# Optimization experiments

Measured on AMD Instinct MI355X. Metric: run time of the kernel, lower is better.

Reference implementation:

```python
import jax, jax.numpy as jnp
import numpy as np

K_NEIGHBORS = 50
DELTA = 0.001


def setup_inputs() -> dict:
    key = jax.random.key(0)
    k1, k2, k3 = jax.random.split(key, 3)
    A, N, D, B = 8, 50000, 64, 256
    return {
        "query": jax.random.normal(k1, (B, D), dtype=jnp.float32),
        "mem_keys": jax.random.normal(k2, (A, N, D), dtype=jnp.float32),
        "mem_values": jax.random.normal(k3, (A, N), dtype=jnp.float32),
    }


def reference(query, mem_keys, mem_values):
    # query: [B, D]; mem_keys: [A, N, D]; mem_values: [A, N]
    q_sq = jnp.sum(query ** 2, axis=-1, keepdims=True)  # [B, 1]

    def per_action(keys, values):
        # keys: [N, D], values: [N]
        # brute-force squared-L2 distances (replaces Annoy ANN search)
        d2 = q_sq + jnp.sum(keys ** 2, axis=-1)[None, :] - 2.0 * query @ keys.T  # [B, N]
        _, idx = jax.lax.top_k(-d2, K_NEIGHBORS)  # [B, K] nearest indices
        gk = keys[idx]        # [B, K, D] gathered keys
        gv = values[idx]      # [B, K]    gathered values
        # inverse-distance kernel, exact recompute as in torch forward
        dist = jnp.sum((query[:, None, :] - gk) ** 2, axis=-1)  # [B, K]
        w = 1.0 / (dist + DELTA)
        out = jnp.sum(w * gv, axis=-1) / jnp.sum(w, axis=-1)  # [B]
        return out, idx, dist

    vals, idxs, scores = jax.vmap(per_action)(mem_keys, mem_values)  # [A,B], [A,B,K], [A,B,K]
    values_all = vals.T  # [B, A]
    max_values = jnp.max(values_all, axis=-1, keepdims=True)   # [B, 1]
    actions = jnp.argmax(values_all, axis=-1, keepdims=True)   # [B, 1]
    return (max_values, actions, values_all,
            jnp.transpose(idxs, (1, 0, 2)), jnp.transpose(scores, (1, 0, 2)))
```

## Files before the change

kernel.cpp:

```cpp
#include <hip/hip_runtime.h>
#include <cstdint>


#define A_N 8
#define N_N 50000
#define D_N 64
#define B_N 256
#define K_N 50

constexpr int   QT  = 64;
constexpr int   NBT = 128;
constexpr int   NT  = (N_N + NBT - 1) / NBT;
constexpr int   SL  = 40;
constexpr int   SLF = 64;
constexpr int   SLOTS = 24;
constexpr int   CAPMAX = 4096;
constexpr float TMARG = 25.0f;
constexpr int   NPAD = NT * NBT;

constexpr int OFF_MAX = 0;
constexpr int OFF_ACT = 256;
constexpr int OFF_VAL = 512;
constexpr int OFF_IDX = 2560;
constexpr int OFF_SC  = 104960;

constexpr size_t WSF_CNT  = 0;
constexpr size_t WSF_THR  = 8192;
constexpr size_t WSF_KBF  = 1609728;
constexpr size_t WSF_CAND = 52858880;

constexpr size_t WS_CNT  = 0;
constexpr size_t WS_QSQ  = 16384;
constexpr size_t WS_KSQ  = 17408;
constexpr size_t WS_CAND = 1617920;

typedef __attribute__((ext_vector_type(8))) short bf16x8;
typedef __attribute__((ext_vector_type(4))) float f32x4;

__device__ __forceinline__ unsigned bfr(float f)
{
    unsigned u = __float_as_uint(f);
    return (u + 0x7FFFu + ((u >> 16) & 1u)) >> 16;
}
__device__ __forceinline__ uint4 packbf8(const float* f)
{
    uint4 w;
    w.x = bfr(f[0]) | (bfr(f[1]) << 16);
    w.y = bfr(f[2]) | (bfr(f[3]) << 16);
    w.z = bfr(f[4]) | (bfr(f[5]) << 16);
    w.w = bfr(f[6]) | (bfr(f[7]) << 16);
    return w;
}

__device__ __forceinline__ void async16(void* lds, const void* g)
{
    __builtin_amdgcn_global_load_lds(
        (const __attribute__((address_space(1))) void*)g,
        (__attribute__((address_space(3))) void*)lds, 16, 0, 0);
}

__device__ __forceinline__ float np_tree8(const float r[8])
{
    return __fadd_rn(__fadd_rn(__fadd_rn(r[0], r[1]), __fadd_rn(r[2], r[3])),
                     __fadd_rn(__fadd_rn(r[4], r[5]), __fadd_rn(r[6], r[7])));
}

__device__ __forceinline__ float np_sumsq64(const float* __restrict__ a)
{
    float r[8];
#pragma unroll
    for (int j = 0; j < 8; ++j) r[j] = __fmul_rn(a[j], a[j]);
    for (int i = 8; i < 64; i += 8)
#pragma unroll
        for (int j = 0; j < 8; ++j)
            r[j] = __fadd_rn(r[j], __fmul_rn(a[i + j], a[i + j]));
    return np_tree8(r);
}

__device__ __forceinline__ float np_sum50(const float* __restrict__ a)
{
    float r[8];
#pragma unroll
    for (int j = 0; j < 8; ++j) r[j] = a[j];
    for (int i = 8; i < 48; i += 8)
#pragma unroll
        for (int j = 0; j < 8; ++j) r[j] = __fadd_rn(r[j], a[i + j]);
    float res = np_tree8(r);
    res = __fadd_rn(res, a[48]);
    res = __fadd_rn(res, a[49]);
    return res;
}


__global__ __launch_bounds__(256)
void dnd_k0b(const float* __restrict__ keys, float* __restrict__ thrn,
             uint4* __restrict__ kbf, int* __restrict__ cnt)
{
    __shared__ float khalf[NBT][2];
    const int t   = blockIdx.x;
    const int a   = blockIdx.y;
    const int tid = threadIdx.x;
    const int r   = tid >> 1, h = tid & 1;

    int n = t * NBT + r; if (n > N_N - 1) n = N_N - 1;
    const float4* s4 = (const float4*)(keys + ((size_t)a * N_N + n) * D_N + h * 32);
    float4 fv[8];
#pragma unroll
    for (int i = 0; i < 8; ++i) fv[i] = s4[i];
    float ps = 0.f;
#pragma unroll
    for (int i = 0; i < 8; ++i)
        ps += fv[i].x * fv[i].x + fv[i].y * fv[i].y + fv[i].z * fv[i].z + fv[i].w * fv[i].w;
    khalf[r][h] = ps;

    const float* f = (const float*)fv;
    const int s = r >> 4, m = r & 15;
    uint4* dst = kbf + ((size_t)(a * NT + t) * 16 + (s * 2 + h)) * 64;
#pragma unroll
    for (int g = 0; g < 4; ++g) dst[g * 16 + m] = packbf8(f + g * 8);

    __syncthreads();
    if (tid < NBT) {
        const int nn = t * NBT + tid;
        float thr = __builtin_huge_valf();
        if (nn < N_N) {
            const float ks = khalf[tid][0] + khalf[tid][1];
            thr = 0.5f * (ks - TMARG);
        }
        thrn[(size_t)a * NPAD + t * NBT + tid] = thr;
    }
    if (t == 0) cnt[a * B_N + tid] = 0;
}

__global__ __launch_bounds__(256, 5)
void dnd_k1(const float* __restrict__ query, const uint4* __restrict__ kbf,
            const float* __restrict__ thrn,
            int* __restrict__ cnt, unsigned* __restrict__ cand, int cap)
{
    __shared__ __align__(16) uint4 afrag[4][2][64];
    __shared__ __align__(16) uint4 bfrag[16][64];
    __shared__ float    thrs[NBT];
    __shared__ int      lcnt[QT];
    __shared__ unsigned lbuf[QT][SLOTS];

    const int a    = blockIdx.z;
    const int q0   = blockIdx.y * QT;
    const int sl   = blockIdx.x;
    const int tid  = threadIdx.x;
    const int lane = tid & 63;
    const int wave = tid >> 6;
    const int quad = lane >> 4;
    const int nl   = lane & 15;

    {
        const int r = tid & 63, seg = tid >> 6;
        const float4* s4 = (const float4*)(query + (size_t)(q0 + r) * D_N + seg * 16);
        float4 fv[4];
#pragma unroll
        for (int i = 0; i < 4; ++i) fv[i] = s4[i];
        const float* f = (const float*)fv;
        const int qtile = r >> 4, m = r & 15, kh = seg >> 1;
        const int quadA = (seg & 1) * 2;
        afrag[qtile][kh][quadA * 16 + m]       = packbf8(f);
        afrag[qtile][kh][(quadA + 1) * 16 + m] = packbf8(f + 8);
    }
    if (tid < QT) lcnt[tid] = 0;
    __syncthreads();
    const bf16x8 aA = ((const bf16x8*)afrag)[(wave * 2 + 0) * 64 + lane];
    const bf16x8 aB = ((const bf16x8*)afrag)[(wave * 2 + 1) * 64 + lane];

    int it = 0;
    for (int t = sl; t < NT; t += SL, ++it) {
        const int n0 = t * NBT;
        __syncthreads();
        {
            const char* src = (const char*)(kbf + (size_t)(a * NT + t) * 1024);
#pragma unroll
            for (int i = 0; i < 4; ++i) {
                const int off = i * 4096 + tid * 16;
                async16((char*)bfrag + off, src + off);
            }
        }
        if (tid < NBT) thrs[tid] = thrn[(size_t)a * NPAD + n0 + tid];
        __syncthreads();

#pragma unroll
        for (int s = 0; s < 8; ++s) {
            const bf16x8 b0 = ((const bf16x8*)bfrag)[(s * 2 + 0) * 64 + lane];
            const bf16x8 b1 = ((const bf16x8*)bfrag)[(s * 2 + 1) * 64 + lane];
            f32x4 c = {0.f, 0.f, 0.f, 0.f};
            c = __builtin_amdgcn_mfma_f32_16x16x32_bf16(aA, b0, c, 0, 0, 0);
            c = __builtin_amdgcn_mfma_f32_16x16x32_bf16(aB, b1, c, 0, 0, 0);

            const int   nn  = n0 + s * 16 + nl;
            const float thr = thrs[s * 16 + nl];
#pragma unroll
            for (int r = 0; r < 4; ++r) {
                if (c[r] >= thr) {
                    const int bl = wave * 16 + quad * 4 + r;
                    const float d2rel = fmaf(-2.f, c[r], fmaf(2.f, thr, TMARG));
                    int qv = (int)fmaf(d2rel, 1000.f, 40000.f);
                    qv = qv < 0 ? 0 : (qv > 65535 ? 65535 : qv);
                    const unsigned entry = ((unsigned)qv << 16) | (unsigned)nn;
                    const int p = atomicAdd(&lcnt[bl], 1);
                    if (p < SLOTS) lbuf[bl][p] = entry;
                    else {
                        const int gb = a * B_N + q0 + bl;
                        const int gp = atomicAdd(&cnt[gb], 1);
                        if (gp < cap) cand[(size_t)gb * cap + gp] = entry;
                    }
                }
            }
        }

        const bool last = (t + SL >= NT);
        if ((it & 1) || last) {
            __syncthreads();
            if (tid < QT) {
                int m = lcnt[tid]; lcnt[tid] = 0;
                if (m > SLOTS) m = SLOTS;
                if (m > 0) {
                    const int gb = a * B_N + q0 + tid;
                    const int base = atomicAdd(&cnt[gb], m);
                    unsigned* dst = cand + (size_t)gb * cap;
                    for (int i = 0; i < m; ++i) {
                        const int p = base + i;
                        if (p < cap) dst[p] = lbuf[tid][i];
                    }
                }
            }
        }
    }
}

__global__ __launch_bounds__(256)
void dnd_k2(const float* __restrict__ query, const float* __restrict__ keys,
            const float* __restrict__ values,
            const int* __restrict__ cnt, const unsigned* __restrict__ cand, int cap,
            float* __restrict__ dout)
{
    __shared__ __align__(16) float qrow[D_N];
    __shared__ int   hist[256];
    __shared__ float sdf[512];
    __shared__ int   sn[512];
    __shared__ int   wn[K_N];
    __shared__ float wsc[K_N];
    __shared__ float wgv[K_N];
    __shared__ int   nsurv;
    __shared__ int   bstar;
    __shared__ float qsq_np;

    const int b   = blockIdx.x;
    const int a   = blockIdx.y;
    const int ab  = a * B_N + b;
    const int tid = threadIdx.x;

    if (tid < D_N) qrow[tid] = query[(size_t)b * D_N + tid];
    hist[tid & 255] = 0;
    if (tid == 0) nsurv = 0;
    if (tid < K_N) wn[tid] = 0;
    __syncthreads();
    if (tid == 0) qsq_np = np_sumsq64(qrow);
    __syncthreads();

    int c = cnt[ab]; if (c > cap) c = cap;
    const unsigned* base = cand + (size_t)ab * cap;

    for (int i = tid; i < c; i += 256) {
        int bin = (int)(base[i] >> 16) / 250;
        bin = bin > 255 ? 255 : bin;
        atomicAdd(&hist[bin], 1);
    }
    __syncthreads();
    if (tid == 0) {
        const int need = c < K_N ? c : K_N;
        int cum = 0, bs = 255;
        for (int i = 0; i < 256; ++i) { cum += hist[i]; if (cum >= need) { bs = i; break; } }
        bstar = bs;
    }
    __syncthreads();
    const int bs = bstar + 4;

    for (int i = tid; i < c; i += 256) {
        const unsigned e = base[i];
        int bin = (int)(e >> 16) / 250;
        bin = bin > 255 ? 255 : bin;
        if (bin <= bs) {
            int p = atomicAdd(&nsurv, 1);
            if (p < 512) sn[p] = (int)(e & 0xFFFFu);
        }
    }
    __syncthreads();
    int c2 = nsurv; if (c2 > 512) c2 = 512;

    const float qn = qsq_np;
    for (int i = tid; i < c2; i += 256) {
        const int n = sn[i];
        const float4* kr = (const float4*)(keys + ((size_t)a * N_N + n) * D_N);
        const float4* qr = (const float4*)qrow;
        float r[8];
#pragma unroll
        for (int j = 0; j < 8; ++j) r[j] = 0.f;
        float dot = 0.f;
#pragma unroll
        for (int cch = 0; cch < 16; ++cch) {
            float4 kk = kr[cch]; float4 qv = qr[cch];
            const int j0 = (cch & 1) * 4;
            if (cch < 2) {
                r[j0 + 0] = __fmul_rn(kk.x, kk.x);
                r[j0 + 1] = __fmul_rn(kk.y, kk.y);
                r[j0 + 2] = __fmul_rn(kk.z, kk.z);
                r[j0 + 3] = __fmul_rn(kk.w, kk.w);
            } else {
                r[j0 + 0] = __fadd_rn(r[j0 + 0], __fmul_rn(kk.x, kk.x));
                r[j0 + 1] = __fadd_rn(r[j0 + 1], __fmul_rn(kk.y, kk.y));
                r[j0 + 2] = __fadd_rn(r[j0 + 2], __fmul_rn(kk.z, kk.z));
                r[j0 + 3] = __fadd_rn(r[j0 + 3], __fmul_rn(kk.w, kk.w));
            }
            dot = __fmaf_rn(qv.x, kk.x, dot);
            dot = __fmaf_rn(qv.y, kk.y, dot);
            dot = __fmaf_rn(qv.z, kk.z, dot);
            dot = __fmaf_rn(qv.w, kk.w, dot);
        }
        const float ksq = np_tree8(r);
        sdf[i] = __fsub_rn(__fadd_rn(qn, ksq), __fmul_rn(2.0f, dot));
    }
    __syncthreads();

    for (int i = tid; i < c2; i += 256) {
        const float di = sdf[i]; const int ni = sn[i];
        int rank = 0;
        for (int j = 0; j < c2; ++j) {
            const float dj = sdf[j]; const int nj = sn[j];
            rank += (dj < di || (dj == di && nj < ni)) ? 1 : 0;
        }
        if (rank < K_N) wn[rank] = ni;
    }
    __syncthreads();

    if (tid < K_N) {
        const int n = wn[tid];
        const float* kr = keys + ((size_t)a * N_N + n) * D_N;
        float r[8];
#pragma unroll
        for (int j = 0; j < 8; ++j) {
            float d = __fsub_rn(qrow[j], kr[j]);
            r[j] = __fmul_rn(d, d);
        }
        for (int i = 8; i < 64; i += 8)
#pragma unroll
            for (int j = 0; j < 8; ++j) {
                float d = __fsub_rn(qrow[i + j], kr[i + j]);
                r[j] = __fadd_rn(r[j], __fmul_rn(d, d));
            }
        const float dist = np_tree8(r);
        wsc[tid] = dist;
        wgv[tid] = values[(size_t)a * N_N + n];
        dout[OFF_IDX + (size_t)(b * A_N + a) * K_N + tid] = (float)n;
        dout[OFF_SC  + (size_t)(b * A_N + a) * K_N + tid] = dist;
    }
    __syncthreads();

    if (tid == 0) {
        float w[K_N], wv[K_N];
#pragma unroll
        for (int k = 0; k < K_N; ++k) {
            w[k]  = __fdiv_rn(1.0f, __fadd_rn(wsc[k], 0.001f));
            wv[k] = __fmul_rn(w[k], wgv[k]);
        }
        dout[OFF_VAL + b * A_N + a] = __fdiv_rn(np_sum50(wv), np_sum50(w));
    }
}

__global__ void dnd_k3(float* __restrict__ dout)
{
    const int b = threadIdx.x;
    float best = -__builtin_huge_valf(); int bi = 0;
#pragma unroll
    for (int a = 0; a < A_N; ++a) {
        const float v = dout[OFF_VAL + b * A_N + a];
        if (v > best) { best = v; bi = a; }
    }
    dout[OFF_MAX + b] = best;
    dout[OFF_ACT + b] = (float)bi;
}


__global__ __launch_bounds__(256)
void dnd_k0f(const float* __restrict__ query, const float* __restrict__ keys,
             float* __restrict__ qsq_g, float* __restrict__ ksq_g)
{
    const int r = blockIdx.x * 256 + threadIdx.x;
    if (r >= A_N * N_N + B_N) return;
    const bool isk = r < A_N * N_N;
    const float4* s4 = (const float4*)(isk ? (keys + (size_t)r * D_N)
                                           : (query + (size_t)(r - A_N * N_N) * D_N));
    float s = 0.f;
#pragma unroll
    for (int i = 0; i < 16; ++i) {
        float4 v = s4[i];
        s += v.x * v.x + v.y * v.y + v.z * v.z + v.w * v.w;
    }
    if (isk) ksq_g[r] = s; else qsq_g[r - A_N * N_N] = s;
}

__global__ __launch_bounds__(256, 4)
void dnd_k1f(const float* __restrict__ query, const float* __restrict__ keys,
             const float* __restrict__ qsq_g, const float* __restrict__ ksq_g,
             int* __restrict__ cnt, uint2* __restrict__ cand, int cap)
{
    __shared__ __align__(16) uint4 afrag[4][2][64];
    __shared__ __align__(16) uint4 bfrag[8][2][64];
    __shared__ float qsqs[QT];
    __shared__ float ksqs[NBT];

    const int a    = blockIdx.z;
    const int q0   = blockIdx.y * QT;
    const int sl   = blockIdx.x;
    const int tid  = threadIdx.x;
    const int lane = tid & 63;
    const int wave = tid >> 6;
    const int quad = lane >> 4;
    const int nl   = lane & 15;

    {
        const int r = tid & 63, seg = tid >> 6;
        const float4* s4 = (const float4*)(query + (size_t)(q0 + r) * D_N + seg * 16);
        float4 fv[4];
#pragma unroll
        for (int i = 0; i < 4; ++i) fv[i] = s4[i];
        const float* f = (const float*)fv;
        const int qtile = r >> 4, m = r & 15, kh = seg >> 1;
        const int quadA = (seg & 1) * 2;
        afrag[qtile][kh][quadA * 16 + m]       = packbf8(f);
        afrag[qtile][kh][(quadA + 1) * 16 + m] = packbf8(f + 8);
    }
    if (tid < QT) qsqs[tid] = qsq_g[q0 + tid];

    for (int t = sl; t < NT; t += SLF) {
        const int n0 = t * NBT;
        __syncthreads();
        {
            const int r = tid >> 1, h = tid & 1;
            int n = n0 + r; if (n > N_N - 1) n = N_N - 1;
            const float4* s4 = (const float4*)(keys + ((size_t)a * N_N + n) * D_N + h * 32);
            float4 fv[8];
#pragma unroll
            for (int i = 0; i < 8; ++i) fv[i] = s4[i];
            const float* f = (const float*)fv;
            const int s = r >> 4, m = r & 15;
#pragma unroll
            for (int g = 0; g < 4; ++g)
                bfrag[s][h][g * 16 + m] = packbf8(f + g * 8);
        }
        if (tid < NBT)
            ksqs[tid] = (n0 + tid < N_N) ? ksq_g[(size_t)a * N_N + n0 + tid]
                                         : __builtin_huge_valf();
        __syncthreads();

        const bf16x8 aA = ((const bf16x8*)afrag)[(wave * 2 + 0) * 64 + lane];
        const bf16x8 aB = ((const bf16x8*)afrag)[(wave * 2 + 1) * 64 + lane];

#pragma unroll
        for (int s = 0; s < 8; ++s) {
            const bf16x8 b0 = ((const bf16x8*)bfrag)[(s * 2 + 0) * 64 + lane];
            const bf16x8 b1 = ((const bf16x8*)bfrag)[(s * 2 + 1) * 64 + lane];
            f32x4 c = {0.f, 0.f, 0.f, 0.f};
            c = __builtin_amdgcn_mfma_f32_16x16x32_bf16(aA, b0, c, 0, 0, 0);
            c = __builtin_amdgcn_mfma_f32_16x16x32_bf16(aB, b1, c, 0, 0, 0);

            const int   nn  = n0 + s * 16 + nl;
            const float ksq = ksqs[s * 16 + nl];
#pragma unroll
            for (int r = 0; r < 4; ++r) {
                const int   qr = wave * 16 + quad * 4 + r;
                const float qq = qsqs[qr];
                const float d2 = qq + ksq - 2.0f * c[r];
                if (d2 <= qq + TMARG) {
                    const int b = q0 + qr;
                    const int p = atomicAdd(&cnt[a * B_N + b], 1);
                    if (p < cap) {
                        uint2 e; e.x = __float_as_uint(d2); e.y = (unsigned)nn;
                        cand[(size_t)(a * B_N + b) * cap + p] = e;
                    }
                }
            }
        }
    }
}

__global__ __launch_bounds__(256, 2)
void dnd_k2f(const float* __restrict__ query, const float* __restrict__ keys,
             const float* __restrict__ values,
             const int* __restrict__ cnt, const uint2* __restrict__ cand, int cap,
             float* __restrict__ dout)
{
    __shared__ __align__(16) float qrow[D_N];
    __shared__ float cd[CAPMAX];
    __shared__ int   cn[CAPMAX];
    __shared__ int   hist[256];
    __shared__ float sdf[512];
    __shared__ int   sn[512];
    __shared__ int   wn[K_N];
    __shared__ float wsc[K_N];
    __shared__ float wgv[K_N];
    __shared__ int   nsurv;
    __shared__ int   bstar;
    __shared__ float sqsq;
    __shared__ float qsq_np;

    const int b   = blockIdx.x;
    const int a   = blockIdx.y;
    const int ab  = a * B_N + b;
    const int tid = threadIdx.x;

    if (tid < D_N) qrow[tid] = query[(size_t)b * D_N + tid];
    hist[tid & 255] = 0;
    if (tid == 0) nsurv = 0;
    if (tid < K_N) wn[tid] = 0;
    __syncthreads();
    if (tid < 64) {
        float v = qrow[tid];
        float s = v * v;
#pragma unroll
        for (int m = 1; m < 64; m <<= 1) s += __shfl_xor(s, m, 64);
        if (tid == 0) sqsq = s;
    }
    if (tid == 0) qsq_np = np_sumsq64(qrow);
    __syncthreads();

    int c = cnt[ab]; if (c > cap) c = cap; if (c > CAPMAX) c = CAPMAX;
    const float qq = sqsq;

    for (int i = tid; i < c; i += 256) {
        uint2 e = cand[(size_t)ab * cap + i];
        float d = __uint_as_float(e.x);
        cd[i] = d; cn[i] = (int)e.y;
        int bin = (int)((d - qq + 40.f) * 4.f);
        bin = bin < 0 ? 0 : (bin > 255 ? 255 : bin);
        atomicAdd(&hist[bin], 1);
    }
    __syncthreads();
    if (tid == 0) {
        const int need = c < K_N ? c : K_N;
        int cum = 0, bs = 255;
        for (int i = 0; i < 256; ++i) { cum += hist[i]; if (cum >= need) { bs = i; break; } }
        bstar = bs;
    }
    __syncthreads();
    const int bs = bstar + 4;

    for (int i = tid; i < c; i += 256) {
        float d = cd[i];
        int bin = (int)((d - qq + 40.f) * 4.f);
        bin = bin < 0 ? 0 : (bin > 255 ? 255 : bin);
        if (bin <= bs) {
            int p = atomicAdd(&nsurv, 1);
            if (p < 512) sn[p] = cn[i];
        }
    }
    __syncthreads();
    int c2 = nsurv; if (c2 > 512) c2 = 512;

    const float qn = qsq_np;
    for (int i = tid; i < c2; i += 256) {
        const int n = sn[i];
        const float4* kr = (const float4*)(keys + ((size_t)a * N_N + n) * D_N);
        const float4* qr = (const float4*)qrow;
        float r[8];
#pragma unroll
        for (int j = 0; j < 8; ++j) r[j] = 0.f;
        float dot = 0.f;
#pragma unroll
        for (int cch = 0; cch < 16; ++cch) {
            float4 kk = kr[cch]; float4 qv = qr[cch];
            const int j0 = (cch & 1) * 4;
            if (cch < 2) {
                r[j0 + 0] = __fmul_rn(kk.x, kk.x);
                r[j0 + 1] = __fmul_rn(kk.y, kk.y);
                r[j0 + 2] = __fmul_rn(kk.z, kk.z);
                r[j0 + 3] = __fmul_rn(kk.w, kk.w);
            } else {
                r[j0 + 0] = __fadd_rn(r[j0 + 0], __fmul_rn(kk.x, kk.x));
                r[j0 + 1] = __fadd_rn(r[j0 + 1], __fmul_rn(kk.y, kk.y));
                r[j0 + 2] = __fadd_rn(r[j0 + 2], __fmul_rn(kk.z, kk.z));
                r[j0 + 3] = __fadd_rn(r[j0 + 3], __fmul_rn(kk.w, kk.w));
            }
            dot = __fmaf_rn(qv.x, kk.x, dot);
            dot = __fmaf_rn(qv.y, kk.y, dot);
            dot = __fmaf_rn(qv.z, kk.z, dot);
            dot = __fmaf_rn(qv.w, kk.w, dot);
        }
        const float ksq = np_tree8(r);
        sdf[i] = __fsub_rn(__fadd_rn(qn, ksq), __fmul_rn(2.0f, dot));
    }
    __syncthreads();

    for (int i = tid; i < c2; i += 256) {
        const float di = sdf[i]; const int ni = sn[i];
        int rank = 0;
        for (int j = 0; j < c2; ++j) {
            const float dj = sdf[j]; const int nj = sn[j];
            rank += (dj < di || (dj == di && nj < ni)) ? 1 : 0;
        }
        if (rank < K_N) wn[rank] = ni;
    }
    __syncthreads();

    if (tid < K_N) {
        const int n = wn[tid];
        const float* kr = keys + ((size_t)a * N_N + n) * D_N;
        float r[8];
#pragma unroll
        for (int j = 0; j < 8; ++j) {
            float d = __fsub_rn(qrow[j], kr[j]);
            r[j] = __fmul_rn(d, d);
        }
        for (int i = 8; i < 64; i += 8)
#pragma unroll
            for (int j = 0; j < 8; ++j) {
                float d = __fsub_rn(qrow[i + j], kr[i + j]);
                r[j] = __fadd_rn(r[j], __fmul_rn(d, d));
            }
        const float dist = np_tree8(r);
        wsc[tid] = dist;
        wgv[tid] = values[(size_t)a * N_N + n];
        dout[OFF_IDX + (size_t)(b * A_N + a) * K_N + tid] = (float)n;
        dout[OFF_SC  + (size_t)(b * A_N + a) * K_N + tid] = dist;
    }
    __syncthreads();

    if (tid == 0) {
        float w[K_N], wv[K_N];
#pragma unroll
        for (int k = 0; k < K_N; ++k) {
            w[k]  = __fdiv_rn(1.0f, __fadd_rn(wsc[k], 0.001f));
            wv[k] = __fmul_rn(w[k], wgv[k]);
        }
        dout[OFF_VAL + b * A_N + a] = __fdiv_rn(np_sum50(wv), np_sum50(w));
    }
}

extern "C" void kernel_launch(void* const* d_in, const int* in_sizes, int n_in,
                              void* d_out, int out_size, void* d_ws, size_t ws_size,
                              hipStream_t stream)
{
    (void)in_sizes; (void)n_in; (void)out_size;
    const float* query  = (const float*)d_in[0];
    const float* keys   = (const float*)d_in[1];
    const float* values = (const float*)d_in[2];
    float* dout = (float*)d_out;
    char*  ws   = (char*)d_ws;

    long long capf = 0;
    if (ws_size > WSF_CAND)
        capf = (long long)((ws_size - WSF_CAND) / ((size_t)A_N * B_N * 4));
    const bool full = capf >= 3072;

    if (full) {
        int cap = capf > CAPMAX ? CAPMAX : (int)capf;
        int*      cnt  = (int*)(ws + WSF_CNT);
        float*    thrn = (float*)(ws + WSF_THR);
        uint4*    kbf  = (uint4*)(ws + WSF_KBF);
        unsigned* cand = (unsigned*)(ws + WSF_CAND);

        dim3 g0(NT, A_N);
        dnd_k0b<<<g0, 256, 0, stream>>>(keys, thrn, kbf, cnt);
        dim3 g1(SL, 4, A_N);
        dnd_k1<<<g1, 256, 0, stream>>>(query, kbf, thrn, cnt, cand, cap);
        dim3 g2(B_N, A_N);
        dnd_k2<<<g2, 256, 0, stream>>>(query, keys, values, cnt, cand, cap, dout);
        dnd_k3<<<1, 256, 0, stream>>>(dout);
    } else {
        int*   cnt   = (int*)(ws + WS_CNT);
        float* qsq_g = (float*)(ws + WS_QSQ);
        float* ksq_g = (float*)(ws + WS_KSQ);
        uint2* cand  = (uint2*)(ws + WS_CAND);
        int cap = CAPMAX;
        if (ws_size > WS_CAND) {
            size_t avail = (ws_size - WS_CAND) / ((size_t)A_N * B_N * 8);
            if ((size_t)cap > avail) cap = (int)avail;
        }
        if (cap < 1) cap = 1;

        hipMemsetAsync(cnt, 0, A_N * B_N * sizeof(int), stream);
        dnd_k0f<<<(A_N * N_N + B_N + 255) / 256, 256, 0, stream>>>(query, keys, qsq_g, ksq_g);
        dim3 g1(SLF, 4, A_N);
        dnd_k1f<<<g1, 256, 0, stream>>>(query, keys, qsq_g, ksq_g, cnt, cand, cap);
        dim3 g2(B_N, A_N);
        dnd_k2f<<<g2, 256, 0, stream>>>(query, keys, values, cnt, cand, cap, dout);
        dnd_k3<<<1, 256, 0, stream>>>(dout);
    }
}
```

Before: 270.9 us.

## Process all 256 queries per block in k1 to reuse key tiles

Each k1 block now holds all 256 queries as bf16 MFMA fragments in registers, instead of 64 queries per block across 4 y-blocks. Every key tile loaded from global memory and LDS therefore feeds 4x more MFMAs, and the grid shrinks to 96 slices by 8 actions. The shared arena is reused: the query fragments occupy it first and the per-query candidate buffers later, with fewer slots per query. In exchange, register pressure rises (launch bounds drop to 3 waves), there are fewer blocks, and more candidates may overflow to global atomics.

After: 284.8 us. 5.1% more time.

```diff
diff --git a/kernel.cpp b/kernel.cpp
--- a/kernel.cpp
+++ b/kernel.cpp
@@ -11,9 +11,9 @@
 constexpr int   QT  = 64;
 constexpr int   NBT = 128;
 constexpr int   NT  = (N_N + NBT - 1) / NBT;
-constexpr int   SL  = 40;
+constexpr int   SLQ = 96;
 constexpr int   SLF = 64;
-constexpr int   SLOTS = 24;
+constexpr int   SLOTSQ = 16;
 constexpr int   CAPMAX = 4096;
 constexpr float TMARG = 25.0f;
 constexpr int   NPAD = NT * NBT;
@@ -132,19 +132,20 @@
     if (t == 0) cnt[a * B_N + tid] = 0;
 }
 
-__global__ __launch_bounds__(256, 5)
+__global__ __launch_bounds__(256, 3)
 void dnd_k1(const float* __restrict__ query, const uint4* __restrict__ kbf,
             const float* __restrict__ thrn,
             int* __restrict__ cnt, unsigned* __restrict__ cand, int cap)
 {
-    __shared__ __align__(16) uint4 afrag[4][2][64];
+    __shared__ __align__(16) char arena[16 * 2 * 64 * 16];
     __shared__ __align__(16) uint4 bfrag[16][64];
-    __shared__ float    thrs[NBT];
-    __shared__ int      lcnt[QT];
-    __shared__ unsigned lbuf[QT][SLOTS];
-
-    const int a    = blockIdx.z;
-    const int q0   = blockIdx.y * QT;
+    __shared__ float thrs[NBT];
+    __shared__ int   lcnt[B_N];
+
+    uint4    (*afrag)[2][64]   = (uint4 (*)[2][64])arena;
+    unsigned (*lbuf)[SLOTSQ]   = (unsigned (*)[SLOTSQ])arena;
+
+    const int a    = blockIdx.y;
     const int sl   = blockIdx.x;
     const int tid  = threadIdx.x;
     const int lane = tid & 63;
@@ -154,23 +155,34 @@
 
     {
         const int r = tid & 63, seg = tid >> 6;
-        const float4* s4 = (const float4*)(query + (size_t)(q0 + r) * D_N + seg * 16);
-        float4 fv[4];
-#pragma unroll
-        for (int i = 0; i < 4; ++i) fv[i] = s4[i];
-        const float* f = (const float*)fv;
-        const int qtile = r >> 4, m = r & 15, kh = seg >> 1;
+        const int m = r & 15, kh = seg >> 1;
         const int quadA = (seg & 1) * 2;
-        afrag[qtile][kh][quadA * 16 + m]       = packbf8(f);
-        afrag[qtile][kh][(quadA + 1) * 16 + m] = packbf8(f + 8);
-    }
-    if (tid < QT) lcnt[tid] = 0;
-    __syncthreads();
-    const bf16x8 aA = ((const bf16x8*)afrag)[(wave * 2 + 0) * 64 + lane];
-    const bf16x8 aB = ((const bf16x8*)afrag)[(wave * 2 + 1) * 64 + lane];
+#pragma unroll
+        for (int rep = 0; rep < 4; ++rep) {
+            const int row = rep * 64 + r;
+            const float4* s4 = (const float4*)(query + (size_t)row * D_N + seg * 16);
+            float4 fv[4];
+#pragma unroll
+            for (int i = 0; i < 4; ++i) fv[i] = s4[i];
+            const float* f = (const float*)fv;
+            const int qt16 = rep * 4 + (r >> 4);
+            afrag[qt16][kh][quadA * 16 + m]       = packbf8(f);
+            afrag[qt16][kh][(quadA + 1) * 16 + m] = packbf8(f + 8);
+        }
+    }
+    lcnt[tid] = 0;
+    __syncthreads();
+
+    bf16x8 aF[4][2];
+#pragma unroll
+    for (int sub = 0; sub < 4; ++sub)
+#pragma unroll
+        for (int kh = 0; kh < 2; ++kh)
+            aF[sub][kh] =
+                ((const bf16x8*)afrag)[((wave * 4 + sub) * 2 + kh) * 64 + lane];
 
     int it = 0;
-    for (int t = sl; t < NT; t += SL, ++it) {
+    for (int t = sl; t < NT; t += SLQ, ++it) {
         const int n0 = t * NBT;
         __syncthreads();
         {
@@ -188,39 +200,41 @@
         for (int s = 0; s < 8; ++s) {
             const bf16x8 b0 = ((const bf16x8*)bfrag)[(s * 2 + 0) * 64 + lane];
             const bf16x8 b1 = ((const bf16x8*)bfrag)[(s * 2 + 1) * 64 + lane];
-            f32x4 c = {0.f, 0.f, 0.f, 0.f};
-            c = __builtin_amdgcn_mfma_f32_16x16x32_bf16(aA, b0, c, 0, 0, 0);
-            c = __builtin_amdgcn_mfma_f32_16x16x32_bf16(aB, b1, c, 0, 0, 0);
-
             const int   nn  = n0 + s * 16 + nl;
             const float thr = thrs[s * 16 + nl];
 #pragma unroll
-            for (int r = 0; r < 4; ++r) {
-                if (c[r] >= thr) {
-                    const int bl = wave * 16 + quad * 4 + r;
-                    const float d2rel = fmaf(-2.f, c[r], fmaf(2.f, thr, TMARG));
-                    int qv = (int)fmaf(d2rel, 1000.f, 40000.f);
-                    qv = qv < 0 ? 0 : (qv > 65535 ? 65535 : qv);
-                    const unsigned entry = ((unsigned)qv << 16) | (unsigned)nn;
-                    const int p = atomicAdd(&lcnt[bl], 1);
-                    if (p < SLOTS) lbuf[bl][p] = entry;
-                    else {
-                        const int gb = a * B_N + q0 + bl;
-                        const int gp = atomicAdd(&cnt[gb], 1);
-                        if (gp < cap) cand[(size_t)gb * cap + gp] = entry;
+            for (int sub = 0; sub < 4; ++sub) {
+                f32x4 c = {0.f, 0.f, 0.f, 0.f};
+                c = __builtin_amdgcn_mfma_f32_16x16x32_bf16(aF[sub][0], b0, c, 0, 0, 0);
+                c = __builtin_amdgcn_mfma_f32_16x16x32_bf16(aF[sub][1], b1, c, 0, 0, 0);
+#pragma unroll
+                for (int r = 0; r < 4; ++r) {
+                    if (c[r] >= thr) {
+                        const int bl = (wave * 4 + sub) * 16 + quad * 4 + r;
+                        const float d2rel = fmaf(-2.f, c[r], fmaf(2.f, thr, TMARG));
+                        int qv = (int)fmaf(d2rel, 1000.f, 40000.f);
+                        qv = qv < 0 ? 0 : (qv > 65535 ? 65535 : qv);
+                        const unsigned entry = ((unsigned)qv << 16) | (unsigned)nn;
+                        const int p = atomicAdd(&lcnt[bl], 1);
+                        if (p < SLOTSQ) lbuf[bl][p] = entry;
+                        else {
+                            const int gb = a * B_N + bl;
+                            const int gp = atomicAdd(&cnt[gb], 1);
+                            if (gp < cap) cand[(size_t)gb * cap + gp] = entry;
+                        }
                     }
                 }
             }
         }
 
-        const bool last = (t + SL >= NT);
+        const bool last = (t + SLQ >= NT);
         if ((it & 1) || last) {
             __syncthreads();
-            if (tid < QT) {
+            {
                 int m = lcnt[tid]; lcnt[tid] = 0;
-                if (m > SLOTS) m = SLOTS;
+                if (m > SLOTSQ) m = SLOTSQ;
                 if (m > 0) {
-                    const int gb = a * B_N + q0 + tid;
+                    const int gb = a * B_N + tid;
                     const int base = atomicAdd(&cnt[gb], m);
                     unsigned* dst = cand + (size_t)gb * cap;
                     for (int i = 0; i < m; ++i) {
@@ -666,7 +680,7 @@
 
         dim3 g0(NT, A_N);
         dnd_k0b<<<g0, 256, 0, stream>>>(keys, thrn, kbf, cnt);
-        dim3 g1(SL, 4, A_N);
+        dim3 g1(SLQ, A_N);
         dnd_k1<<<g1, 256, 0, stream>>>(query, kbf, thrn, cnt, cand, cap);
         dim3 g2(B_N, A_N);
         dnd_k2<<<g2, 256, 0, stream>>>(query, keys, values, cnt, cand, cap, dout);
```

## Double-buffer key tiles in candidate kernel and load query fragments into registers

Applied to the files above, without the earlier changes.

The candidate-filter kernel now uses two LDS buffers for key tiles and thresholds. While the current tile is being processed with MFMA, the next tile is prefetched asynchronously into the other buffer, which removes the second barrier per iteration. Query A-fragments are loaded and packed straight into registers instead of going through LDS. Slice count per (action, query-tile) drops from 40 to 32 and occupancy is lowered to 4 blocks per CU, which gives more tiles per block in exchange for the larger LDS footprint and fewer concurrent blocks.

Result: slower. 279.5 us (+3.2%).

```diff
diff --git a/kernel.cpp b/kernel.cpp
--- a/kernel.cpp
+++ b/kernel.cpp
@@ -11,7 +11,7 @@
 constexpr int   QT  = 64;
 constexpr int   NBT = 128;
 constexpr int   NT  = (N_N + NBT - 1) / NBT;
-constexpr int   SL  = 40;
+constexpr int   SL  = 32;
 constexpr int   SLF = 64;
 constexpr int   SLOTS = 24;
 constexpr int   CAPMAX = 4096;
@@ -132,14 +132,13 @@
     if (t == 0) cnt[a * B_N + tid] = 0;
 }
 
-__global__ __launch_bounds__(256, 5)
+__global__ __launch_bounds__(256, 4)
 void dnd_k1(const float* __restrict__ query, const uint4* __restrict__ kbf,
             const float* __restrict__ thrn,
             int* __restrict__ cnt, unsigned* __restrict__ cand, int cap)
 {
-    __shared__ __align__(16) uint4 afrag[4][2][64];
-    __shared__ __align__(16) uint4 bfrag[16][64];
-    __shared__ float    thrs[NBT];
+    __shared__ __align__(16) uint4 bfrag[2][16][64];
+    __shared__ __align__(16) float thrs[2][NBT];
     __shared__ int      lcnt[QT];
     __shared__ unsigned lbuf[QT][SLOTS];
 
@@ -152,48 +151,62 @@
     const int quad = lane >> 4;
     const int nl   = lane & 15;
 
+    bf16x8 aA, aB;
     {
-        const int r = tid & 63, seg = tid >> 6;
-        const float4* s4 = (const float4*)(query + (size_t)(q0 + r) * D_N + seg * 16);
-        float4 fv[4];
-#pragma unroll
-        for (int i = 0; i < 4; ++i) fv[i] = s4[i];
-        const float* f = (const float*)fv;
-        const int qtile = r >> 4, m = r & 15, kh = seg >> 1;
-        const int quadA = (seg & 1) * 2;
-        afrag[qtile][kh][quadA * 16 + m]       = packbf8(f);
-        afrag[qtile][kh][(quadA + 1) * 16 + m] = packbf8(f + 8);
+        const float* qb = query + (size_t)(q0 + wave * 16 + nl) * D_N + quad * 8;
+        float f0[8], f1[8];
+        *(float4*)(f0)     = *(const float4*)(qb);
+        *(float4*)(f0 + 4) = *(const float4*)(qb + 4);
+        *(float4*)(f1)     = *(const float4*)(qb + 32);
+        *(float4*)(f1 + 4) = *(const float4*)(qb + 36);
+        uint4 pa = packbf8(f0), pb = packbf8(f1);
+        aA = *(bf16x8*)&pa;
+        aB = *(bf16x8*)&pb;
     }
     if (tid < QT) lcnt[tid] = 0;
-    __syncthreads();
-    const bf16x8 aA = ((const bf16x8*)afrag)[(wave * 2 + 0) * 64 + lane];
-    const bf16x8 aB = ((const bf16x8*)afrag)[(wave * 2 + 1) * 64 + lane];
-
-    int it = 0;
+
+    {
+        const char* src = (const char*)(kbf + (size_t)(a * NT + sl) * 1024);
+        char* dst = (char*)&bfrag[0][0][0];
+#pragma unroll
+        for (int i = 0; i < 4; ++i) {
+            const int off = i * 4096 + tid * 16;
+            async16(dst + off, src + off);
+        }
+        if (tid < 32)
+            async16((char*)&thrs[0][0] + tid * 16,
+                    (const char*)(thrn + (size_t)a * NPAD + sl * NBT) + tid * 16);
+    }
+
+    int cur = 0, it = 0;
     for (int t = sl; t < NT; t += SL, ++it) {
-        const int n0 = t * NBT;
         __syncthreads();
-        {
-            const char* src = (const char*)(kbf + (size_t)(a * NT + t) * 1024);
+
+        const int tn = t + SL;
+        if (tn < NT) {
+            const char* src = (const char*)(kbf + (size_t)(a * NT + tn) * 1024);
+            char* dst = (char*)&bfrag[cur ^ 1][0][0];
 #pragma unroll
             for (int i = 0; i < 4; ++i) {
                 const int off = i * 4096 + tid * 16;
-                async16((char*)bfrag + off, src + off);
+                async16(dst + off, src + off);
             }
-        }
-        if (tid < NBT) thrs[tid] = thrn[(size_t)a * NPAD + n0 + tid];
-        __syncthreads();
-
+            if (tid < 32)
+                async16((char*)&thrs[cur ^ 1][0] + tid * 16,
+                        (const char*)(thrn + (size_t)a * NPAD + tn * NBT) + tid * 16);
+        }
+
+        const int n0 = t * NBT;
 #pragma unroll
         for (int s = 0; s < 8; ++s) {
-            const bf16x8 b0 = ((const bf16x8*)bfrag)[(s * 2 + 0) * 64 + lane];
-            const bf16x8 b1 = ((const bf16x8*)bfrag)[(s * 2 + 1) * 64 + lane];
+            const bf16x8 b0 = ((const bf16x8*)bfrag[cur])[(s * 2 + 0) * 64 + lane];
+            const bf16x8 b1 = ((const bf16x8*)bfrag[cur])[(s * 2 + 1) * 64 + lane];
             f32x4 c = {0.f, 0.f, 0.f, 0.f};
             c = __builtin_amdgcn_mfma_f32_16x16x32_bf16(aA, b0, c, 0, 0, 0);
             c = __builtin_amdgcn_mfma_f32_16x16x32_bf16(aB, b1, c, 0, 0, 0);
 
             const int   nn  = n0 + s * 16 + nl;
-            const float thr = thrs[s * 16 + nl];
+            const float thr = thrs[cur][s * 16 + nl];
 #pragma unroll
             for (int r = 0; r < 4; ++r) {
                 if (c[r] >= thr) {
@@ -230,6 +243,7 @@
                 }
             }
         }
+        cur ^= 1;
     }
 }
 
```
